# Optimization experiments

Measured on AMD Instinct MI355X. Metric: run time of the kernel, lower is better.

The kernel has to match this reference:

```python
import jax, jax.numpy as jnp
import numpy as np

B, T, C = 1, 2048, 1024
H = 16
HD = C // H
BLOCK = 2048
NEG = float('-inf')

def setup_inputs() -> dict:
    key = jax.random.key(0)
    ks = jax.random.split(key, 6)
    x = jax.random.normal(ks[0], (B, T, C), dtype=jnp.float32)
    cumulative_scores = jax.random.normal(ks[1], (B, T), dtype=jnp.float32) * 0.1
    padding_mask = jnp.ones((B, T), dtype=jnp.float32)
    token_index = jax.random.randint(ks[2], (B, T), 0, BLOCK).astype(jnp.int64)
    w_attn = jax.random.normal(ks[3], (C, 3 * C), dtype=jnp.float32) * (1.0 / np.sqrt(C))
    b_attn = jnp.zeros((3 * C,), dtype=jnp.float32)
    w_proj = jax.random.normal(ks[4], (C, C), dtype=jnp.float32) * (1.0 / np.sqrt(C))
    b_proj = jnp.zeros((C,), dtype=jnp.float32)
    return dict(x=x, cumulative_scores=cumulative_scores, padding_mask=padding_mask,
                token_index=token_index, w_attn=w_attn, b_attn=b_attn,
                w_proj=w_proj, b_proj=b_proj)

def _rotate_half(z):
    z1, z2 = z[..., : z.shape[-1] // 2], z[..., z.shape[-1] // 2 :]
    return jnp.concatenate((-z2, z1), axis=-1)

def reference(x, cumulative_scores, padding_mask, token_index, w_attn, b_attn, w_proj, b_proj):
    # fused QKV projection
    qkv = x @ w_attn + b_attn                      # (B,T,3C)
    q, k, v = jnp.split(qkv, 3, axis=2)
    q = q.reshape(B, T, H, HD).transpose(0, 2, 1, 3)  # (B,H,T,HD)
    k = k.reshape(B, T, H, HD).transpose(0, 2, 1, 3)
    v = v.reshape(B, T, H, HD).transpose(0, 2, 1, 3)

    # dynamic per-token RoPE positions: global token counts (original scatter
    # broadcasts indices over batch, so counts are global across all batches)
    cnt = jnp.zeros((BLOCK,), jnp.float32).at[token_index.reshape(-1)].add(1.0)
    per_tok = (1.0 / (cnt + 1e-10))[token_index]       # (B,T)
    partial = jnp.cumsum(per_tok, axis=-1)             # (B,T) fractional positions

    inv_freq = 1.0 / (10000.0 ** (jnp.arange(0, HD, 2, dtype=jnp.float32) / HD))
    freqs = partial[..., None] * inv_freq              # (B,T,HD/2)
    emb = jnp.concatenate((freqs, freqs), axis=-1)     # (B,T,HD)
    cos = jnp.cos(emb)[:, None]                        # (B,1,T,HD)
    sin = jnp.sin(emb)[:, None]
    q = q * cos + _rotate_half(q) * sin
    k = k * cos + _rotate_half(k) * sin

    # 'fork' plan: overwrite last channel
    q = q.at[..., -1].set(1.0)
    k = k.at[..., -1].set(jnp.broadcast_to(cumulative_scores[:, None, :], (B, H, T)))

    # additive causal + padding mask (B,T,T)
    causal = jnp.where(jnp.tril(jnp.ones((T, T), jnp.bool_)), 0.0, NEG)
    pm = jnp.take_along_axis(padding_mask, token_index, axis=1)     # (B,T)
    outer = pm[:, :, None] * pm[:, None, :]
    pad_add = jnp.where(outer.astype(jnp.bool_), 0.0, NEG)
    mask = causal[None, :, :] + pad_add                              # (B,T,T)

    # scale v by exp(cumulative_scores)
    v = v * jnp.exp(cumulative_scores)[:, None, :, None]

    scores = jnp.einsum('bhqd,bhkd->bhqk', q, k) / np.sqrt(HD) + mask[:, None]
    probs = jax.nn.softmax(scores, axis=-1)
    y = jnp.einsum('bhqk,bhkd->bhqd', probs, v)        # (B,H,T,HD)
    y = y.transpose(0, 2, 1, 3).reshape(B, T, C)
    return y @ w_proj + b_proj
```

## Files before the change

### kernel.cpp

```cpp
#include <hip/hip_runtime.h>
#include <math.h>

#define T 2048
#define C 1024
#define H 16
#define HD 64
#define N3 (3*C)
#define NBLOCK 2048

typedef __attribute__((ext_vector_type(8))) short bf16x8;
typedef __attribute__((ext_vector_type(4))) float f32x4;

#define MFMA16(a, b, c) __builtin_amdgcn_mfma_f32_16x16x32_bf16((a), (b), (c), 0, 0, 0)

__device__ inline short f2bf(float f) {
    unsigned u; __builtin_memcpy(&u, &f, 4);
    unsigned r = (u + 0x7fffu + ((u >> 16) & 1u)) >> 16;
    return (short)r;
}
__device__ inline float bf2f(short s) {
    unsigned u = ((unsigned)(unsigned short)s) << 16;
    float f; __builtin_memcpy(&f, &u, 4);
    return f;
}

__device__ inline void gload_lds16(const void* g, void* l) {
    __builtin_amdgcn_global_load_lds((const __attribute__((address_space(1))) unsigned int*)g,
                                     (__attribute__((address_space(3))) unsigned int*)l,
                                     16, 0, 0);
}

__global__ __launch_bounds__(256) void pre_kernel(const float* __restrict__ x,
                                                  const float* __restrict__ w_attn,
                                                  const float* __restrict__ w_proj,
                                                  const int* __restrict__ tok,
                                                  const float* __restrict__ padmask,
                                                  short* __restrict__ xb,
                                                  short* __restrict__ wabT,
                                                  short* __restrict__ wpbT,
                                                  float* __restrict__ partial,
                                                  float* __restrict__ pm_tok) {
    int bid = blockIdx.x;
    int tid = threadIdx.x;
    if (bid == 3072) {
        __shared__ float cntS[NBLOCK];
        __shared__ float sums[256];
        #pragma unroll
        for (int j = 0; j < 8; ++j) cntS[tid * 8 + j] = 0.0f;
        __syncthreads();
        int tk[8];
        #pragma unroll
        for (int j = 0; j < 8; ++j) {
            tk[j] = tok[tid * 8 + j];
            atomicAdd(&cntS[tk[j]], 1.0f);
        }
        __syncthreads();
        float vals[8];
        float s = 0.0f;
        #pragma unroll
        for (int j = 0; j < 8; ++j) {
            s += 1.0f / (cntS[tk[j]] + 1e-10f);
            vals[j] = s;
            pm_tok[tid * 8 + j] = padmask[tk[j]];
        }
        sums[tid] = s;
        __syncthreads();
        for (int off = 1; off < 256; off <<= 1) {
            float v = (tid >= off) ? sums[tid - off] : 0.0f;
            __syncthreads();
            sums[tid] += v;
            __syncthreads();
        }
        float offset = (tid > 0) ? sums[tid - 1] : 0.0f;
        #pragma unroll
        for (int j = 0; j < 8; ++j) partial[tid * 8 + j] = offset + vals[j];
        return;
    }
    if (bid < 2048) {
        int i = bid * 1024 + tid * 4;
        float4 v = *(const float4*)(x + i);
        short4 o;
        o.x = f2bf(v.x); o.y = f2bf(v.y); o.z = f2bf(v.z); o.w = f2bf(v.w);
        *(short4*)(xb + i) = o;
        return;
    }
    __shared__ float S[64][65];
    const float* in; short* out; int Kd, Nd, bx, by;
    if (bid < 2816) {
        int b = bid - 2048;
        bx = b % 48; by = b / 48;
        in = w_attn; out = wabT; Kd = C; Nd = N3;
    } else {
        int b = bid - 2816;
        bx = b % 16; by = b / 16;
        in = w_proj; out = wpbT; Kd = C; Nd = C;
    }
    int n0 = bx * 64, k0 = by * 64;
    #pragma unroll
    for (int i = 0; i < 16; ++i) {
        int lin = tid + i * 256;
        int r = lin >> 6, c = lin & 63;
        S[r][c] = in[(size_t)(k0 + r) * Nd + n0 + c];
    }
    __syncthreads();
    #pragma unroll
    for (int i = 0; i < 16; ++i) {
        int lin = tid + i * 256;
        int rn = lin >> 6, ck = lin & 63;
        out[(size_t)(n0 + rn) * Kd + k0 + ck] = f2bf(S[ck][rn]);
    }
}

template <int OUT_BF16, int BNF>
__global__ __launch_bounds__(256) void gemm_bt(const short* __restrict__ A,
                                               const short* __restrict__ Bt,
                                               const float* __restrict__ bias,
                                               void* __restrict__ Cout,
                                               int M, int N, int K) {
    constexpr int BN = BNF * 32;
    __shared__ alignas(16) short As[2][128 * 32];
    __shared__ alignas(16) short Bs[2][BN * 32];
    int tid = threadIdx.x;
    int m0 = blockIdx.y * 128, n0 = blockIdx.x * BN;
    int w = tid >> 6, l = tid & 63;
    int wm = (w >> 1) * 64, wn = (w & 1) * (BNF * 16);
    int lq = l & 15, g = l >> 4;
    int prow = l >> 2, pcol = (l & 3) * 8;
    f32x4 acc[4][BNF] = {};

    auto stage = [&](int buf, int k0) {
        #pragma unroll
        for (int i = 0; i < 2; ++i) {
            int c = w * 2 + i;
            int row = c * 16 + prow;
            gload_lds16(A + (size_t)(m0 + row) * K + k0 + pcol, As[buf] + c * 512);
        }
        #pragma unroll
        for (int i = 0; i < BNF / 2; ++i) {
            int c = w * (BNF / 2) + i;
            int row = c * 16 + prow;
            gload_lds16(Bt + (size_t)(n0 + row) * K + k0 + pcol, Bs[buf] + c * 512);
        }
    };

    int NK = K / 32;
    stage(0, 0);
    asm volatile("s_waitcnt vmcnt(0)" ::: "memory");
    __builtin_amdgcn_s_barrier();
    __builtin_amdgcn_sched_barrier(0);

    for (int t = 0; t < NK; ++t) {
        int cur = t & 1;
        if (t + 1 < NK) stage(cur ^ 1, (t + 1) * 32);

        bf16x8 af[4], bfr[BNF];
        #pragma unroll
        for (int f = 0; f < 4; ++f)
            af[f] = *(const bf16x8*)(As[cur] + (wm + f * 16 + lq) * 32 + g * 8);
        #pragma unroll
        for (int j = 0; j < BNF; ++j)
            bfr[j] = *(const bf16x8*)(Bs[cur] + (wn + j * 16 + lq) * 32 + g * 8);
        __builtin_amdgcn_s_setprio(1);
        #pragma unroll
        for (int fi = 0; fi < 4; ++fi)
            #pragma unroll
            for (int fj = 0; fj < BNF; ++fj)
                acc[fi][fj] = MFMA16(af[fi], bfr[fj], acc[fi][fj]);
        __builtin_amdgcn_s_setprio(0);

        asm volatile("s_waitcnt vmcnt(0)" ::: "memory");
        __builtin_amdgcn_s_barrier();
        __builtin_amdgcn_sched_barrier(0);
    }

    #pragma unroll
    for (int fi = 0; fi < 4; ++fi)
        #pragma unroll
        for (int fj = 0; fj < BNF; ++fj)
            #pragma unroll
            for (int r = 0; r < 4; ++r) {
                int m = m0 + wm + fi * 16 + g * 4 + r;
                int n = n0 + wn + fj * 16 + lq;
                float v = acc[fi][fj][r] + bias[n];
                if (OUT_BF16) ((short*)Cout)[(size_t)m * N + n] = f2bf(v);
                else          ((float*)Cout)[(size_t)m * N + n] = v;
            }
}

__global__ __launch_bounds__(256) void ropevt(short* __restrict__ qkvb,
                                              const float* __restrict__ partial,
                                              const float* __restrict__ cumsc,
                                              const float* __restrict__ pm_tok,
                                              short* __restrict__ vbT) {
    __shared__ alignas(16) short S[64][72];
    __shared__ float efs[64];
    int bid = blockIdx.x;
    int tid = threadIdx.x;
    if (bid < 512) {
        int tg = tid >> 6, l = tid & 63;
        int t = bid * 4 + tg;
        int j = l & 31;
        float inv = exp2f(-(float)j * (13.287712379549449f / 32.0f));
        float ang = partial[t] * inv;
        float cs_own = cosf(ang), sn_own = sinf(ang);
        float csc = cumsc[t];
        float pmv = pm_tok[t];
        float qfix = (pmv != 0.0f) ? 1.0f : 0.0f;
        float kfix = (pmv != 0.0f) ? csc : -1e20f;

        int h = l >> 2, jb = (l & 3) * 8;
        short* row = qkvb + (size_t)t * N3;
        int c1 = h * 64 + jb;
        bf16x8 qlo = *(const bf16x8*)(row + c1);
        bf16x8 qhi = *(const bf16x8*)(row + c1 + 32);
        bf16x8 klo = *(const bf16x8*)(row + C + c1);
        bf16x8 khi = *(const bf16x8*)(row + C + c1 + 32);
        bf16x8 qlo2, qhi2, klo2, khi2;
        #pragma unroll
        for (int i = 0; i < 8; ++i) {
            float cs = __shfl(cs_own, jb + i);
            float sn = __shfl(sn_own, jb + i);
            float q1 = bf2f(qlo[i]), q2 = bf2f(qhi[i]);
            float k1 = bf2f(klo[i]), k2 = bf2f(khi[i]);
            float q2n = q2 * cs + q1 * sn;
            float k2n = k2 * cs + k1 * sn;
            if (jb + i == 31) { q2n = qfix; k2n = kfix; }
            qlo2[i] = f2bf(q1 * cs - q2 * sn);
            qhi2[i] = f2bf(q2n);
            klo2[i] = f2bf(k1 * cs - k2 * sn);
            khi2[i] = f2bf(k2n);
        }
        *(bf16x8*)(row + c1) = qlo2;
        *(bf16x8*)(row + c1 + 32) = qhi2;
        *(bf16x8*)(row + C + c1) = klo2;
        *(bf16x8*)(row + C + c1 + 32) = khi2;
        return;
    }
    int b = bid - 512;
    int h = b >> 5;
    int t0 = (b & 31) * 64;
    if (tid < 64) efs[tid] = __expf(cumsc[t0 + tid]);
    __syncthreads();
    #pragma unroll
    for (int e = 0; e < 2; ++e) {
        int s = tid * 2 + e;
        int r = s >> 3, c8 = (s & 7) * 8;
        bf16x8 v = *(const bf16x8*)(qkvb + (size_t)(t0 + r) * N3 + 2 * C + h * 64 + c8);
        float ef = efs[r];
        bf16x8 o;
        #pragma unroll
        for (int i = 0; i < 8; ++i) o[i] = f2bf(bf2f(v[i]) * ef);
        *(bf16x8*)&S[r][c8] = o;
    }
    __syncthreads();
    #pragma unroll
    for (int e = 0; e < 2; ++e) {
        int s = tid * 2 + e;
        int d = s >> 3, t8 = (s & 7) * 8;
        bf16x8 o;
        #pragma unroll
        for (int i = 0; i < 8; ++i) o[i] = S[t8 + i][d];
        *(bf16x8*)(vbT + (size_t)(h * 64 + d) * T + t0 + t8) = o;
    }
}

__global__ __launch_bounds__(256) void attn_flash(const short* __restrict__ qkvb,
                                                  const short* __restrict__ vbT,
                                                  short* __restrict__ yb) {
    __shared__ alignas(16) short Kt[2][64 * 64];
    __shared__ alignas(16) short Vt[2][64 * 64];
    __shared__ alignas(16) short Ps[4][16][72];

    int b = blockIdx.x;
    int h, qt;
    if (b < 256) { h = b & 15; qt = 31 - (b >> 4); }
    else         { int c2 = b - 256; h = c2 & 15; qt = c2 >> 4; }
    int tid = threadIdx.x;
    int w = tid >> 6, l = tid & 63;
    int lq = l & 15, g = l >> 4;
    int qrl = w * 16 + lq;

    const short* qbase = qkvb + (size_t)(qt * 64 + qrl) * N3 + h * 64;
    bf16x8 qf0 = *(const bf16x8*)(qbase + g * 8);
    bf16x8 qf1 = *(const bf16x8*)(qbase + 32 + g * 8);

    f32x4 accO[4] = {};
    float lsum = 0.0f;

    int srow = tid >> 3, scol = (tid & 7) * 8;
    const short* kgb = qkvb + C + h * 64 + scol;
    const short* vgb = vbT + (size_t)(h * 64) * T + scol;
    int wb0 = srow * 128 + ((scol * 2) ^ ((srow & 7) << 4));
    int wb1 = (srow + 32) * 128 + ((scol * 2) ^ ((srow & 7) << 4));

    auto do_tile = [&](int cur, bool masked) {
        const char* Kc = (const char*)Kt[cur];
        const char* Vc = (const char*)Vt[cur];
        f32x4 s[4] = {};
        __builtin_amdgcn_s_setprio(1);
        #pragma unroll
        for (int f = 0; f < 4; ++f) {
            int row = f * 16 + lq;
            const char* kr_ = Kc + row * 128;
            int sw = (row & 7) << 4;
            bf16x8 a0 = *(const bf16x8*)(kr_ + ((g * 16) ^ sw));
            bf16x8 a1 = *(const bf16x8*)(kr_ + ((64 + g * 16) ^ sw));
            s[f] = MFMA16(a0, qf0, s[f]);
            s[f] = MFMA16(a1, qf1, s[f]);
        }
        __builtin_amdgcn_s_setprio(0);
        float p[16];
        #pragma unroll
        for (int f = 0; f < 4; ++f)
            #pragma unroll
            for (int r = 0; r < 4; ++r) {
                float sv = s[f][r] * 0.125f;
                if (masked) {
                    int kl = f * 16 + g * 4 + r;
                    sv = (kl > qrl) ? -INFINITY : sv;
                }
                float pv = __expf(sv);
                p[f * 4 + r] = pv;
                lsum += pv;
            }
        #pragma unroll
        for (int f = 0; f < 4; ++f) {
            unsigned u0, u1;
            asm("v_cvt_pk_bf16_f32 %0, %1, %2" : "=v"(u0) : "v"(p[f * 4 + 0]), "v"(p[f * 4 + 1]));
            asm("v_cvt_pk_bf16_f32 %0, %1, %2" : "=v"(u1) : "v"(p[f * 4 + 2]), "v"(p[f * 4 + 3]));
            uint2 uu; uu.x = u0; uu.y = u1;
            *(uint2*)&Ps[w][lq][f * 16 + g * 4] = uu;
        }
        __builtin_amdgcn_s_setprio(1);
        #pragma unroll
        for (int kh = 0; kh < 2; ++kh) {
            bf16x8 pa = *(const bf16x8*)&Ps[w][lq][kh * 32 + g * 8];
            #pragma unroll
            for (int f = 0; f < 4; ++f) {
                int vrow = f * 16 + lq;
                const char* vr_ = Vc + vrow * 128;
                bf16x8 vb = *(const bf16x8*)(vr_ + (((kh * 32 + g * 8) * 2) ^ ((vrow & 7) << 4)));
                accO[f] = MFMA16(pa, vb, accO[f]);
            }
        }
        __builtin_amdgcn_s_setprio(0);
    };

    uint4 kr0 = *(const uint4*)(kgb + (size_t)srow * N3);
    uint4 kr1 = *(const uint4*)(kgb + (size_t)(srow + 32) * N3);
    uint4 vr0 = *(const uint4*)(vgb + (size_t)srow * T);
    uint4 vr1 = *(const uint4*)(vgb + (size_t)(srow + 32) * T);
    *(uint4*)((char*)Kt[0] + wb0) = kr0;
    *(uint4*)((char*)Kt[0] + wb1) = kr1;
    *(uint4*)((char*)Vt[0] + wb0) = vr0;
    *(uint4*)((char*)Vt[0] + wb1) = vr1;
    __syncthreads();

    for (int t = 0; t < qt; ++t) {
        int kn = (t + 1) * 64;
        kr0 = *(const uint4*)(kgb + (size_t)(kn + srow) * N3);
        kr1 = *(const uint4*)(kgb + (size_t)(kn + srow + 32) * N3);
        vr0 = *(const uint4*)(vgb + (size_t)srow * T + kn);
        vr1 = *(const uint4*)(vgb + (size_t)(srow + 32) * T + kn);

        do_tile(t & 1, false);

        int nxt = (t & 1) ^ 1;
        *(uint4*)((char*)Kt[nxt] + wb0) = kr0;
        *(uint4*)((char*)Kt[nxt] + wb1) = kr1;
        *(uint4*)((char*)Vt[nxt] + wb0) = vr0;
        *(uint4*)((char*)Vt[nxt] + wb1) = vr1;
        __syncthreads();
    }
    do_tile(qt & 1, true);

    lsum += __shfl_xor(lsum, 16);
    lsum += __shfl_xor(lsum, 32);
    float linv_own = 1.0f / lsum;
    float li[4];
    #pragma unroll
    for (int r = 0; r < 4; ++r) li[r] = __shfl(linv_own, g * 4 + r);

    #pragma unroll
    for (int f = 0; f < 4; ++f)
        #pragma unroll
        for (int r = 0; r < 4; ++r) {
            int trow = qt * 64 + w * 16 + g * 4 + r;
            yb[(size_t)trow * C + h * 64 + f * 16 + lq] = f2bf(accO[f][r] * li[r]);
        }
}

extern "C" void kernel_launch(void* const* d_in, const int* in_sizes, int n_in,
                              void* d_out, int out_size, void* d_ws, size_t ws_size,
                              hipStream_t stream) {
    const float* x       = (const float*)d_in[0];
    const float* cumsc   = (const float*)d_in[1];
    const float* padmask = (const float*)d_in[2];
    const int*   tok     = (const int*)d_in[3];
    const float* w_attn  = (const float*)d_in[4];
    const float* b_attn  = (const float*)d_in[5];
    const float* w_proj  = (const float*)d_in[6];
    const float* b_proj  = (const float*)d_in[7];
    float* out = (float*)d_out;

    float* part   = (float*)d_ws;
    float* pm_tok = part + 2048;
    short* xb     = (short*)(pm_tok + 2048);
    short* wabT   = xb + (size_t)T * C;
    short* wpbT   = wabT + (size_t)N3 * C;
    short* qkvb   = wpbT + (size_t)C * C;
    short* vbT    = qkvb + (size_t)T * N3;
    short* yb     = vbT + (size_t)C * T;

    pre_kernel<<<3073, 256, 0, stream>>>(x, w_attn, w_proj, tok, padmask,
                                         xb, wabT, wpbT, part, pm_tok);
    gemm_bt<1, 4><<<dim3(N3 / 128, T / 128), 256, 0, stream>>>(xb, wabT, b_attn, qkvb, T, N3, C);
    ropevt<<<1024, 256, 0, stream>>>(qkvb, part, cumsc, pm_tok, vbT);
    attn_flash<<<512, 256, 0, stream>>>(qkvb, vbT, yb);
    gemm_bt<0, 2><<<dim3(C / 64, T / 128), 256, 0, stream>>>(yb, wpbT, b_proj, out, T, C, C);
}
```

Measured before the change: 91.46 us.

## Fuse RoPE and V-transpose into QKV GEMM epilogue with swizzled 128x64 tiles

Removes the separate ropevt kernel. RoPE rotation, the fork last-channel overwrite, and the exp-scaled V transpose now run inside the QKV GEMM epilogue, using a cos/sin table precomputed in the pre-kernel's single scan block. The GEMM is rewritten as a 128x64 tile with K-step 64 and an XOR-swizzled LDS layout to avoid bank conflicts. This saves a launch and a read-modify-write pass over qkv. In exchange, the single scan block now computes 64K sincos values serially, which may lengthen the pre-kernel's critical path. The QKV GEMM grid also changes from 24x16 to 48x16 blocks.

```diff
diff --git a/kernel.cpp b/kernel.cpp
--- a/kernel.cpp
+++ b/kernel.cpp
@@ -38,7 +38,7 @@
                                                   short* __restrict__ xb,
                                                   short* __restrict__ wabT,
                                                   short* __restrict__ wpbT,
-                                                  float* __restrict__ partial,
+                                                  float2* __restrict__ tab,
                                                   float* __restrict__ pm_tok) {
     int bid = blockIdx.x;
     int tid = threadIdx.x;
@@ -72,8 +72,21 @@
             __syncthreads();
         }
         float offset = (tid > 0) ? sums[tid - 1] : 0.0f;
-        #pragma unroll
-        for (int j = 0; j < 8; ++j) partial[tid * 8 + j] = offset + vals[j];
+        float invf[32];
+        #pragma unroll
+        for (int j = 0; j < 32; ++j)
+            invf[j] = exp2f(-(float)j * (13.287712379549449f / 32.0f));
+        #pragma unroll
+        for (int e = 0; e < 8; ++e) {
+            float p = offset + vals[e];
+            float2* row = tab + (tid * 8 + e) * 32;
+            #pragma unroll
+            for (int j = 0; j < 32; ++j) {
+                float s_, c_;
+                __sincosf(p * invf[j], &s_, &c_);
+                row[j] = make_float2(c_, s_);
+            }
+        }
         return;
     }
     if (bid < 2048) {
@@ -111,39 +124,41 @@
     }
 }
 
-template <int OUT_BF16, int BNF>
-__global__ __launch_bounds__(256) void gemm_bt(const short* __restrict__ A,
-                                               const short* __restrict__ Bt,
-                                               const float* __restrict__ bias,
-                                               void* __restrict__ Cout,
-                                               int M, int N, int K) {
-    constexpr int BN = BNF * 32;
-    __shared__ alignas(16) short As[2][128 * 32];
-    __shared__ alignas(16) short Bs[2][BN * 32];
+template <int EPI>
+__global__ __launch_bounds__(256) void gemm128x64(const short* __restrict__ A,
+                                                  const short* __restrict__ Bt,
+                                                  const float* __restrict__ bias,
+                                                  void* __restrict__ Cout,
+                                                  int N, int K,
+                                                  const float2* __restrict__ tab,
+                                                  const float* __restrict__ cumsc,
+                                                  const float* __restrict__ pm_tok,
+                                                  short* __restrict__ vbT) {
+    __shared__ alignas(16) short As[2][128 * 64];
+    __shared__ alignas(16) short Bs[2][64 * 64];
     int tid = threadIdx.x;
-    int m0 = blockIdx.y * 128, n0 = blockIdx.x * BN;
+    int m0 = blockIdx.y * 128, n0 = blockIdx.x * 64;
     int w = tid >> 6, l = tid & 63;
-    int wm = (w >> 1) * 64, wn = (w & 1) * (BNF * 16);
     int lq = l & 15, g = l >> 4;
-    int prow = l >> 2, pcol = (l & 3) * 8;
-    f32x4 acc[4][BNF] = {};
+    int urow = l >> 3;
+    int sw_col = ((l & 7) ^ urow) * 8;
+
+    f32x4 acc[2][4] = {};
 
     auto stage = [&](int buf, int k0) {
         #pragma unroll
+        for (int i = 0; i < 4; ++i) {
+            int u = w * 4 + i;
+            gload_lds16(A + (size_t)(m0 + u * 8 + urow) * K + k0 + sw_col, As[buf] + u * 512);
+        }
+        #pragma unroll
         for (int i = 0; i < 2; ++i) {
-            int c = w * 2 + i;
-            int row = c * 16 + prow;
-            gload_lds16(A + (size_t)(m0 + row) * K + k0 + pcol, As[buf] + c * 512);
-        }
-        #pragma unroll
-        for (int i = 0; i < BNF / 2; ++i) {
-            int c = w * (BNF / 2) + i;
-            int row = c * 16 + prow;
-            gload_lds16(Bt + (size_t)(n0 + row) * K + k0 + pcol, Bs[buf] + c * 512);
+            int u = w * 2 + i;
+            gload_lds16(Bt + (size_t)(n0 + u * 8 + urow) * K + k0 + sw_col, Bs[buf] + u * 512);
         }
     };
 
-    int NK = K / 32;
+    int NK = K / 64;
     stage(0, 0);
     asm volatile("s_waitcnt vmcnt(0)" ::: "memory");
     __builtin_amdgcn_s_barrier();
@@ -151,116 +166,102 @@
 
     for (int t = 0; t < NK; ++t) {
         int cur = t & 1;
-        if (t + 1 < NK) stage(cur ^ 1, (t + 1) * 32);
-
-        bf16x8 af[4], bfr[BNF];
-        #pragma unroll
-        for (int f = 0; f < 4; ++f)
-            af[f] = *(const bf16x8*)(As[cur] + (wm + f * 16 + lq) * 32 + g * 8);
-        #pragma unroll
-        for (int j = 0; j < BNF; ++j)
-            bfr[j] = *(const bf16x8*)(Bs[cur] + (wn + j * 16 + lq) * 32 + g * 8);
-        __builtin_amdgcn_s_setprio(1);
-        #pragma unroll
-        for (int fi = 0; fi < 4; ++fi)
-            #pragma unroll
-            for (int fj = 0; fj < BNF; ++fj)
-                acc[fi][fj] = MFMA16(af[fi], bfr[fj], acc[fi][fj]);
-        __builtin_amdgcn_s_setprio(0);
-
+        if (t + 1 < NK) stage(cur ^ 1, (t + 1) * 64);
+        #pragma unroll
+        for (int kk = 0; kk < 2; ++kk) {
+            bf16x8 af[2], bfr[4];
+            #pragma unroll
+            for (int fi = 0; fi < 2; ++fi) {
+                int rd = w * 32 + fi * 16 + lq;
+                af[fi] = *(const bf16x8*)(As[cur] + rd * 64 + (((kk * 4 + g) ^ (rd & 7)) * 8));
+            }
+            #pragma unroll
+            for (int fj = 0; fj < 4; ++fj) {
+                int rd = fj * 16 + lq;
+                bfr[fj] = *(const bf16x8*)(Bs[cur] + rd * 64 + (((kk * 4 + g) ^ (rd & 7)) * 8));
+            }
+            __builtin_amdgcn_s_setprio(1);
+            #pragma unroll
+            for (int fi = 0; fi < 2; ++fi)
+                #pragma unroll
+                for (int fj = 0; fj < 4; ++fj)
+                    acc[fi][fj] = MFMA16(af[fi], bfr[fj], acc[fi][fj]);
+            __builtin_amdgcn_s_setprio(0);
+        }
         asm volatile("s_waitcnt vmcnt(0)" ::: "memory");
         __builtin_amdgcn_s_barrier();
         __builtin_amdgcn_sched_barrier(0);
     }
 
-    #pragma unroll
-    for (int fi = 0; fi < 4; ++fi)
-        #pragma unroll
-        for (int fj = 0; fj < BNF; ++fj)
+    if (EPI == 0) {
+        float* Cf = (float*)Cout;
+        #pragma unroll
+        for (int fi = 0; fi < 2; ++fi)
             #pragma unroll
             for (int r = 0; r < 4; ++r) {
-                int m = m0 + wm + fi * 16 + g * 4 + r;
-                int n = n0 + wn + fj * 16 + lq;
-                float v = acc[fi][fj][r] + bias[n];
-                if (OUT_BF16) ((short*)Cout)[(size_t)m * N + n] = f2bf(v);
-                else          ((float*)Cout)[(size_t)m * N + n] = v;
-            }
-}
-
-__global__ __launch_bounds__(256) void ropevt(short* __restrict__ qkvb,
-                                              const float* __restrict__ partial,
-                                              const float* __restrict__ cumsc,
-                                              const float* __restrict__ pm_tok,
-                                              short* __restrict__ vbT) {
-    __shared__ alignas(16) short S[64][72];
-    __shared__ float efs[64];
-    int bid = blockIdx.x;
-    int tid = threadIdx.x;
-    if (bid < 512) {
-        int tg = tid >> 6, l = tid & 63;
-        int t = bid * 4 + tg;
-        int j = l & 31;
-        float inv = exp2f(-(float)j * (13.287712379549449f / 32.0f));
-        float ang = partial[t] * inv;
-        float cs_own = cosf(ang), sn_own = sinf(ang);
-        float csc = cumsc[t];
-        float pmv = pm_tok[t];
-        float qfix = (pmv != 0.0f) ? 1.0f : 0.0f;
-        float kfix = (pmv != 0.0f) ? csc : -1e20f;
-
-        int h = l >> 2, jb = (l & 3) * 8;
-        short* row = qkvb + (size_t)t * N3;
-        int c1 = h * 64 + jb;
-        bf16x8 qlo = *(const bf16x8*)(row + c1);
-        bf16x8 qhi = *(const bf16x8*)(row + c1 + 32);
-        bf16x8 klo = *(const bf16x8*)(row + C + c1);
-        bf16x8 khi = *(const bf16x8*)(row + C + c1 + 32);
-        bf16x8 qlo2, qhi2, klo2, khi2;
-        #pragma unroll
-        for (int i = 0; i < 8; ++i) {
-            float cs = __shfl(cs_own, jb + i);
-            float sn = __shfl(sn_own, jb + i);
-            float q1 = bf2f(qlo[i]), q2 = bf2f(qhi[i]);
-            float k1 = bf2f(klo[i]), k2 = bf2f(khi[i]);
-            float q2n = q2 * cs + q1 * sn;
-            float k2n = k2 * cs + k1 * sn;
-            if (jb + i == 31) { q2n = qfix; k2n = kfix; }
-            qlo2[i] = f2bf(q1 * cs - q2 * sn);
-            qhi2[i] = f2bf(q2n);
-            klo2[i] = f2bf(k1 * cs - k2 * sn);
-            khi2[i] = f2bf(k2n);
-        }
-        *(bf16x8*)(row + c1) = qlo2;
-        *(bf16x8*)(row + c1 + 32) = qhi2;
-        *(bf16x8*)(row + C + c1) = klo2;
-        *(bf16x8*)(row + C + c1 + 32) = khi2;
-        return;
-    }
-    int b = bid - 512;
-    int h = b >> 5;
-    int t0 = (b & 31) * 64;
-    if (tid < 64) efs[tid] = __expf(cumsc[t0 + tid]);
-    __syncthreads();
-    #pragma unroll
-    for (int e = 0; e < 2; ++e) {
-        int s = tid * 2 + e;
-        int r = s >> 3, c8 = (s & 7) * 8;
-        bf16x8 v = *(const bf16x8*)(qkvb + (size_t)(t0 + r) * N3 + 2 * C + h * 64 + c8);
-        float ef = efs[r];
-        bf16x8 o;
-        #pragma unroll
-        for (int i = 0; i < 8; ++i) o[i] = f2bf(bf2f(v[i]) * ef);
-        *(bf16x8*)&S[r][c8] = o;
-    }
-    __syncthreads();
-    #pragma unroll
-    for (int e = 0; e < 2; ++e) {
-        int s = tid * 2 + e;
-        int d = s >> 3, t8 = (s & 7) * 8;
-        bf16x8 o;
-        #pragma unroll
-        for (int i = 0; i < 8; ++i) o[i] = S[t8 + i][d];
-        *(bf16x8*)(vbT + (size_t)(h * 64 + d) * T + t0 + t8) = o;
+                int m = m0 + w * 32 + fi * 16 + g * 4 + r;
+                #pragma unroll
+                for (int fj = 0; fj < 4; ++fj) {
+                    int n = n0 + fj * 16 + lq;
+                    Cf[(size_t)m * N + n] = acc[fi][fj][r] + bias[n];
+                }
+            }
+    } else {
+        short* Cb = (short*)Cout;
+        int nt = n0 >> 6;
+        if (nt < 32) {
+            bool isQ = (nt < 16);
+            #pragma unroll
+            for (int fi = 0; fi < 2; ++fi)
+                #pragma unroll
+                for (int r = 0; r < 4; ++r) {
+                    int trow = m0 + w * 32 + fi * 16 + g * 4 + r;
+                    float pm = pm_tok[trow];
+                    float csc = cumsc[trow];
+                    float2 cs0 = tab[trow * 32 + lq];
+                    float2 cs1 = tab[trow * 32 + 16 + lq];
+                    float a0 = acc[fi][0][r] + bias[n0 + lq];
+                    float a1 = acc[fi][1][r] + bias[n0 + 16 + lq];
+                    float a2 = acc[fi][2][r] + bias[n0 + 32 + lq];
+                    float a3 = acc[fi][3][r] + bias[n0 + 48 + lq];
+                    float lo0 = a0 * cs0.x - a2 * cs0.y;
+                    float hi0 = a2 * cs0.x + a0 * cs0.y;
+                    float lo1 = a1 * cs1.x - a3 * cs1.y;
+                    float hi1 = a3 * cs1.x + a1 * cs1.y;
+                    if (lq == 15)
+                        hi1 = isQ ? ((pm != 0.0f) ? 1.0f : 0.0f)
+                                  : ((pm != 0.0f) ? csc : -1e20f);
+                    size_t base = (size_t)trow * N3 + n0;
+                    Cb[base + lq]      = f2bf(lo0);
+                    Cb[base + 16 + lq] = f2bf(lo1);
+                    Cb[base + 32 + lq] = f2bf(hi0);
+                    Cb[base + 48 + lq] = f2bf(hi1);
+                }
+        } else {
+            int h = nt - 32;
+            short* Sv = &As[0][0];
+            __syncthreads();
+            #pragma unroll
+            for (int fi = 0; fi < 2; ++fi)
+                #pragma unroll
+                for (int r = 0; r < 4; ++r) {
+                    int tloc = w * 32 + fi * 16 + g * 4 + r;
+                    float ef = __expf(cumsc[m0 + tloc]);
+                    #pragma unroll
+                    for (int fj = 0; fj < 4; ++fj) {
+                        int d = fj * 16 + lq;
+                        Sv[d * 136 + tloc] = f2bf((acc[fi][fj][r] + bias[n0 + d]) * ef);
+                    }
+                }
+            __syncthreads();
+            #pragma unroll
+            for (int e = 0; e < 4; ++e) {
+                int idx = tid * 4 + e;
+                int d = idx >> 4, t8 = (idx & 15) * 8;
+                bf16x8 o = *(const bf16x8*)(Sv + d * 136 + t8);
+                *(bf16x8*)(vbT + (size_t)(h * 64 + d) * T + m0 + t8) = o;
+            }
+        }
     }
 }
 
@@ -403,19 +404,20 @@
     const float* b_proj  = (const float*)d_in[7];
     float* out = (float*)d_out;
 
-    float* part   = (float*)d_ws;
-    float* pm_tok = part + 2048;
-    short* xb     = (short*)(pm_tok + 2048);
-    short* wabT   = xb + (size_t)T * C;
-    short* wpbT   = wabT + (size_t)N3 * C;
-    short* qkvb   = wpbT + (size_t)C * C;
-    short* vbT    = qkvb + (size_t)T * N3;
-    short* yb     = vbT + (size_t)C * T;
+    float*  pm_tok = (float*)d_ws;
+    float2* tab    = (float2*)(pm_tok + 2048);
+    short*  xb     = (short*)(pm_tok + 2048 + 131072);
+    short*  wabT   = xb + (size_t)T * C;
+    short*  wpbT   = wabT + (size_t)N3 * C;
+    short*  qkvb   = wpbT + (size_t)C * C;
+    short*  vbT    = qkvb + (size_t)T * N3;
+    short*  yb     = vbT + (size_t)C * T;
 
     pre_kernel<<<3073, 256, 0, stream>>>(x, w_attn, w_proj, tok, padmask,
-                                         xb, wabT, wpbT, part, pm_tok);
-    gemm_bt<1, 4><<<dim3(N3 / 128, T / 128), 256, 0, stream>>>(xb, wabT, b_attn, qkvb, T, N3, C);
-    ropevt<<<1024, 256, 0, stream>>>(qkvb, part, cumsc, pm_tok, vbT);
+                                         xb, wabT, wpbT, tab, pm_tok);
+    gemm128x64<1><<<dim3(48, 16), 256, 0, stream>>>(xb, wabT, b_attn, qkvb, N3, C,
+                                                    tab, cumsc, pm_tok, vbT);
     attn_flash<<<512, 256, 0, stream>>>(qkvb, vbT, yb);
-    gemm_bt<0, 2><<<dim3(C / 64, T / 128), 256, 0, stream>>>(yb, wpbT, b_proj, out, T, C, C);
-}
+    gemm128x64<0><<<dim3(16, 16), 256, 0, stream>>>(yb, wpbT, b_proj, out, C, C,
+                                                    nullptr, nullptr, nullptr, nullptr);
+}
```

Result: slower. 94.67 us (+3.5%).
